# Kernel tuning notes

Hardware: AMD Instinct MI355X
Metric: run time of the kernel (lower is better)

The kernel has to match this reference:

```python
import jax, jax.numpy as jnp
import numpy as np

SQRT_HALF = np.float32(1.0 / np.sqrt(2.0))

# ---------- symmetric-extension index helpers (match dtcwt reflect/symm_pad) ----------

def _reflect(x, minx, maxx):
    rng = maxx - minx
    mod = np.fmod(x - minx, 2 * rng)
    mod = np.where(mod < 0, mod + 2 * rng, mod)
    out = np.where(mod >= rng, 2 * rng - mod, mod) + minx
    return out.astype(np.int64)

def _symm_pad(l, m):
    # indices -m .. l+m-1 reflected with half-sample symmetry (edge repeated)
    return _reflect(np.arange(-m, l + m), -0.5, l - 0.5)

# ---------- 1-D filtering along rows (filters are pre-reversed, so correlation == convolution) ----------

def _corr_rows(X, h):
    # X: (N, C, Hp, W); h: (k,) traced; valid cross-correlation along axis 2
    k = h.shape[0]
    n = X.shape[2] - k + 1
    acc = h[0] * X[:, :, :n, :]
    for t in range(1, k):
        acc = acc + h[t] * X[:, :, t:t + n, :]
    return acc

def colfilter(X, h):
    # level-1 (biort) column filter, symmetric extension, same-size output
    m = h.shape[0] // 2
    xe = _symm_pad(X.shape[2], m)
    return _corr_rows(X[:, :, xe, :], h)

def rowfilter(X, h):
    return jnp.swapaxes(colfilter(jnp.swapaxes(X, 2, 3), h), 2, 3)

def colifilt(X, ha, hb, highpass=False):
    # qshift interpolated column filter: upsample rows by 2 using the (ha, hb) tree pair.
    # Faithful to pytorch_wavelets lowlevel.colifilt (filters stored reversed by prep_filt).
    m = ha.shape[0]
    m2 = m // 2
    r = X.shape[2]  # must be even
    xe = _symm_pad(r, m2)
    hao, hae = ha[1::2], ha[::2]
    hbo, hbe = hb[1::2], hb[::2]
    if m2 % 2 == 0:
        taps = (hae, hbe, hao, hbo)
        if highpass:
            idx = (xe[1:-2:2], xe[:-2:2], xe[3::2], xe[2::2])
        else:
            idx = (xe[:-2:2], xe[1:-2:2], xe[2::2], xe[3::2])
    else:
        taps = (hao, hbo, hae, hbe)
        if highpass:
            idx = (xe[2:-1:2], xe[1:-1:2], xe[2:-1:2], xe[1:-1:2])
        else:
            idx = (xe[1:-1:2], xe[2:-1:2], xe[1:-1:2], xe[2:-1:2])
    ys = [_corr_rows(X[:, :, i, :], h) for i, h in zip(idx, taps)]
    N, C, r2, W = ys[0].shape  # r2 == r // 2
    # interleave the 4 phases -> 2*r rows
    return jnp.stack(ys, axis=3).reshape(N, C, 4 * r2, W)

def rowifilt(X, ha, hb, highpass=False):
    return jnp.swapaxes(colifilt(jnp.swapaxes(X, 2, 3), ha, hb, highpass), 2, 3)


def c2q(w1, w2):
    # w1, w2: (N, C, H, W, 2) -> (N, C, 2H, 2W)
    w1r, w1i = w1[..., 0], w1[..., 1]
    w2r, w2i = w2[..., 0], w2[..., 1]
    a = (w1r + w2r) * SQRT_HALF
    b = (w1i + w2i) * SQRT_HALF
    c = (w1i - w2i) * SQRT_HALF
    d = (w2r - w1r) * SQRT_HALF
    N, C, H, W = a.shape
    top = jnp.stack([a, b], axis=-1).reshape(N, C, H, 2 * W)
    bot = jnp.stack([c, d], axis=-1).reshape(N, C, H, 2 * W)
    return jnp.stack([top, bot], axis=3).reshape(N, C, 2 * H, 2 * W)

# ---------- per-level inverse synthesis ----------

def _inv_j1(ll, yh, g0o, g1o):
    lh = c2q(yh[:, :, 0], yh[:, :, 5])  # 15 / 165 deg
    hl = c2q(yh[:, :, 2], yh[:, :, 3])  # 75 / 105 deg
    hh = c2q(yh[:, :, 1], yh[:, :, 4])  # 45 / 135 deg
    y1 = colfilter(ll, g0o) + colfilter(lh, g1o)
    y2 = colfilter(hl, g0o) + colfilter(hh, g1o)
    return rowfilter(y1, g0o) + rowfilter(y2, g1o)

def _inv_j2plus(ll, yh, g0a, g0b, g1a, g1b):
    lh = c2q(yh[:, :, 0], yh[:, :, 5])
    hl = c2q(yh[:, :, 2], yh[:, :, 3])
    hh = c2q(yh[:, :, 1], yh[:, :, 4])
    y1 = colifilt(ll, g0b, g0a) + colifilt(lh, g1b, g1a, True)
    y2 = colifilt(hl, g0b, g0a) + colifilt(hh, g1b, g1a, True)
    return rowifilt(y1, g0b, g0a) + rowifilt(y2, g1b, g1a, True)

# ---------- filters (near_sym_a biort + qshift_a 10-tap synthesis filters) ----------

def _filters():
    g0o = np.array([-3., -15., 73., 170., 73., -15., -3.]) / 280.0  # 7-tap synthesis lowpass
    g1o = np.array([-1., -5., 12., -5., -1.]) / 20.0                # 5-tap synthesis highpass
    q = np.array([0.03516384, 0.0, -0.08832942, 0.23389032, 0.76027237,
                  0.58751830, 0.0, -0.11430184, 0.0, 0.0])          # 10-tap qshift prototype
    alt = (-1.0) ** np.arange(10)
    g0a, g0b = q[::-1].copy(), q.copy()
    g1a = (alt * q[::-1]).copy()
    g1b = (-alt * q).copy()
    # prep_filt reverses filters so cross-correlation implements true convolution
    f32 = lambda h: jnp.asarray(np.ascontiguousarray(h[::-1]), dtype=jnp.float32)
    return {"g0o": f32(g0o), "g1o": f32(g1o), "g0a": f32(g0a),
            "g0b": f32(g0b), "g1a": f32(g1a), "g1b": f32(g1b)}

def setup_inputs() -> dict:
    key = jax.random.key(0)
    k1, k2, k3, k4 = jax.random.split(key, 4)
    N, C, H = 4, 16, 512  # reconstruct 512x512, J=3
    inp = {
        "yl":  jax.random.normal(k1, (N, C, H // 4, H // 4), jnp.float32),
        "yh0": jax.random.normal(k2, (N, C, 6, H // 2, H // 2, 2), jnp.float32),
        "yh1": jax.random.normal(k3, (N, C, 6, H // 4, H // 4, 2), jnp.float32),
        "yh2": jax.random.normal(k4, (N, C, 6, H // 8, H // 8, 2), jnp.float32),
    }
    inp.update(_filters())
    return inp

def reference(yl, yh0, yh1, yh2, g0o, g1o, g0a, g0b, g1a, g1b):
    ll = _inv_j2plus(yl, yh2, g0a, g0b, g1a, g1b)   # 128 -> 256
    ll = _inv_j2plus(ll, yh1, g0a, g0b, g1a, g1b)   # 256 -> 512
    return _inv_j1(ll, yh0, g0o, g1o)               # 512 -> 512
```

## Files before the change

### kernel.cpp

```cpp
#include <hip/hip_runtime.h>
#include <hip/hip_fp16.h>

#define SQH 0.70710678118654752440f
#define NC 64

typedef float nfloat4 __attribute__((ext_vector_type(4)));

template<int L>
static __device__ __forceinline__ int refl(int i) {
    int j = i & (2 * L - 1);
    return (j >= L) ? (2 * L - 1 - j) : j;
}

static __device__ __forceinline__ void c2q_quad4(float4 A, float4 B,
                                                 float4& p0, float4& p1) {
    p0 = make_float4(SQH * (A.x + B.x), SQH * (A.y + B.y),
                     SQH * (A.z + B.z), SQH * (A.w + B.w));
    p1 = make_float4(SQH * (A.y - B.y), SQH * (B.x - A.x),
                     SQH * (A.w - B.w), SQH * (B.z - A.z));
}

static __device__ __forceinline__ void fma4(float4& a, float s, float4 v) {
    a.x += s * v.x; a.y += s * v.y; a.z += s * v.z; a.w += s * v.w;
}

static __device__ __forceinline__ float4 ld4(const float* p, size_t i4) {
    return ((const float4*)p)[i4];
}
static __device__ __forceinline__ float4 ld4(const __half* p, size_t i4) {
    const __half2* h = (const __half2*)p;
    float2 lo = __half22float2(h[2 * i4]);
    float2 hi = __half22float2(h[2 * i4 + 1]);
    return make_float4(lo.x, lo.y, hi.x, hi.y);
}
static __device__ __forceinline__ void st4(float* p, size_t i4, float4 v) {
    ((float4*)p)[i4] = v;
}
static __device__ __forceinline__ void st4(__half* p, size_t i4, float4 v) {
    __half2* h = (__half2*)p;
    h[2 * i4]     = __float22half2_rn(make_float2(v.x, v.y));
    h[2 * i4 + 1] = __float22half2_rn(make_float2(v.z, v.w));
}

template<int R_, int W_, int TY, typename InT, typename OutT>
__global__ __launch_bounds__(256) void k_i(const InT* __restrict__ ll,
                                           const float* __restrict__ yh,
                                           OutT* __restrict__ out,
                                           const float* __restrict__ g0a, const float* __restrict__ g0b,
                                           const float* __restrict__ g1a, const float* __restrict__ g1b) {
    constexpr int RH = R_ / 2, WH = W_ / 2, WQ = W_ / 4;
    constexpr int SLABS = 2 * R_ / TY;
    constexpr int SW = W_ + 12;
    __shared__ float Y1[TY][SW], Y2[TY][SW];

    constexpr int NBLK = SLABS * NC;
    int bid = blockIdx.x;
    int idx = (bid & 7) * (NBLK >> 3) + (bid >> 3);
    int nc = idx / SLABS, slab = idx % SLABS;
    int nc6 = nc * 6;
    int R0 = slab * TY, i0 = R0 >> 2;
    bool edge = (slab == 0) || (slab == SLABS - 1);

    const InT* llp = ll + (size_t)nc * R_ * W_;
    const float4* yh4 = (const float4*)yh;
    const float4* pHLa = yh4 + (size_t)(nc6 + 2) * RH * WQ;
    const float4* pHLb = yh4 + (size_t)(nc6 + 3) * RH * WQ;
    const float4* pLHa = yh4 + (size_t)(nc6 + 0) * RH * WQ;
    const float4* pLHb = yh4 + (size_t)(nc6 + 5) * RH * WQ;
    const float4* pHHa = yh4 + (size_t)(nc6 + 1) * RH * WQ;
    const float4* pHHb = yh4 + (size_t)(nc6 + 4) * RH * WQ;

    constexpr int ATASK = WQ * (TY / 4);
    for (int task = threadIdx.x; task < ATASK; task += 256) {
        int jq = task & (WQ - 1);
        int gl = task / WQ;
        int i  = i0 + gl;

        float4 a10 = {0,0,0,0}, a20 = {0,0,0,0}, a11 = {0,0,0,0}, a21 = {0,0,0,0};
        float4 a12 = {0,0,0,0}, a22 = {0,0,0,0}, a13 = {0,0,0,0}, a23 = {0,0,0,0};
#pragma unroll
        for (int t = 0; t < 5; ++t) {
            float4 lE, lO, hlE, hlO, lhE, lhO, hhE, hhO;
            if (edge) {
                int rE = refl<R_>(2 * i - 4 + 2 * t);
                int rO = refl<R_>(2 * i - 3 + 2 * t);
                lE = ld4(llp, (size_t)rE * WQ + jq);
                lO = ld4(llp, (size_t)rO * WQ + jq);
                int ii = rE >> 1, diE = rE & 1;
                size_t off = (size_t)ii * WQ + jq;
                float4 p0, p1;
                c2q_quad4(pHLa[off], pHLb[off], p0, p1);
                hlE = diE ? p1 : p0;  hlO = diE ? p0 : p1;
                c2q_quad4(pLHa[off], pLHb[off], p0, p1);
                lhE = diE ? p1 : p0;  lhO = diE ? p0 : p1;
                c2q_quad4(pHHa[off], pHHb[off], p0, p1);
                hhE = diE ? p1 : p0;  hhO = diE ? p0 : p1;
            } else {
                lE = ld4(llp, (size_t)(2 * i - 4 + 2 * t) * WQ + jq);
                lO = ld4(llp, (size_t)(2 * i - 3 + 2 * t) * WQ + jq);
                size_t off = (size_t)(i - 2 + t) * WQ + jq;
                c2q_quad4(pHLa[off], pHLb[off], hlE, hlO);
                c2q_quad4(pLHa[off], pLHb[off], lhE, lhO);
                c2q_quad4(pHHa[off], pHHb[off], hhE, hhO);
            }
            float b0o = g0b[2 * t + 1], a0o = g0a[2 * t + 1];
            float b0e = g0b[2 * t],     a0e = g0a[2 * t];
            float b1o = g1b[2 * t + 1], a1o = g1a[2 * t + 1];
            float b1e = g1b[2 * t],     a1e = g1a[2 * t];
            fma4(a10, b0o, lE);  fma4(a10, b1o, lhO);
            fma4(a20, b0o, hlE); fma4(a20, b1o, hhO);
            fma4(a11, a0o, lO);  fma4(a11, a1o, lhE);
            fma4(a21, a0o, hlO); fma4(a21, a1o, hhE);
            fma4(a12, b0e, lE);  fma4(a12, b1e, lhO);
            fma4(a22, b0e, hlE); fma4(a22, b1e, hhO);
            fma4(a13, a0e, lO);  fma4(a13, a1e, lhE);
            fma4(a23, a0e, hlO); fma4(a23, a1e, hhE);
        }
        int rl = 4 * gl, xc = 4 * jq + 4;
        *(float4*)&Y1[rl + 0][xc] = a10;  *(float4*)&Y2[rl + 0][xc] = a20;
        *(float4*)&Y1[rl + 1][xc] = a11;  *(float4*)&Y2[rl + 1][xc] = a21;
        *(float4*)&Y1[rl + 2][xc] = a12;  *(float4*)&Y2[rl + 2][xc] = a22;
        *(float4*)&Y1[rl + 3][xc] = a13;  *(float4*)&Y2[rl + 3][xc] = a23;
    }
    __syncthreads();

    for (int t = threadIdx.x; t < TY * 9; t += 256) {
        int r = t / 9, h = t % 9;
        int dst, src;
        if (h < 4) { dst = h;              src = 7 - h; }
        else       { int k = h - 4; dst = 4 + W_ + k; src = 4 + W_ - 1 - k; }
        Y1[r][dst] = Y1[r][src];
        Y2[r][dst] = Y2[r][src];
    }
    __syncthreads();

    constexpr int QW = W_ / 2;
    for (int task = threadIdx.x; task < TY * QW; task += 256) {
        int j = task & (QW - 1);
        int r = task / QW;
        float2 v1[5], v2[5];
#pragma unroll
        for (int t = 0; t < 5; ++t) {
            v1[t] = *(const float2*)&Y1[r][2 * j + 2 * t];
            v2[t] = *(const float2*)&Y2[r][2 * j + 2 * t];
        }
        float4 o = make_float4(0.f, 0.f, 0.f, 0.f);
#pragma unroll
        for (int t = 0; t < 5; ++t) {
            float b0o = g0b[2 * t + 1], a0o = g0a[2 * t + 1];
            float b0e = g0b[2 * t],     a0e = g0a[2 * t];
            float b1o = g1b[2 * t + 1], a1o = g1a[2 * t + 1];
            float b1e = g1b[2 * t],     a1e = g1a[2 * t];
            o.x += b0o * v1[t].x + b1o * v2[t].y;
            o.y += a0o * v1[t].y + a1o * v2[t].x;
            o.z += b0e * v1[t].x + b1e * v2[t].y;
            o.w += a0e * v1[t].y + a1e * v2[t].x;
        }
        st4(out, (size_t)(nc * 2 * R_ + R0 + r) * QW + j, o);
    }
}

template<int H, int W, int TY, typename InT>
__global__ __launch_bounds__(256) void k_f0(const InT* __restrict__ ll,
                                            const float* __restrict__ yh,
                                            float* __restrict__ out,
                                            const float* __restrict__ g0o,
                                            const float* __restrict__ g1o) {
    constexpr int RH = H / 2, WH = W / 2, WQ = W / 4;
    constexpr int SLABS = H / TY;
    constexpr int SW = W + 12;
    __shared__ float Y1[TY][SW], Y2[TY][SW];

    constexpr int NBLK = SLABS * NC;
    int bid = blockIdx.x;
    int idx = (bid & 7) * (NBLK >> 3) + (bid >> 3);
    int nc = idx / SLABS, slab = idx % SLABS;
    int nc6 = nc * 6;
    int r0 = slab * TY;
    bool edge = (slab == 0) || (slab == SLABS - 1);

    const InT* llp = ll + (size_t)nc * H * W;
    const float4* yh4 = (const float4*)yh;
    const float4* pHLa = yh4 + (size_t)(nc6 + 2) * RH * WQ;
    const float4* pHLb = yh4 + (size_t)(nc6 + 3) * RH * WQ;
    const float4* pLHa = yh4 + (size_t)(nc6 + 0) * RH * WQ;
    const float4* pLHb = yh4 + (size_t)(nc6 + 5) * RH * WQ;
    const float4* pHHa = yh4 + (size_t)(nc6 + 1) * RH * WQ;
    const float4* pHHb = yh4 + (size_t)(nc6 + 4) * RH * WQ;

    float f0[7], f1[5];
#pragma unroll
    for (int k = 0; k < 7; ++k) f0[k] = g0o[k];
#pragma unroll
    for (int k = 0; k < 5; ++k) f1[k] = g1o[k];

    constexpr int ATASK = WQ * (TY / 4);
    for (int task = threadIdx.x; task < ATASK; task += 256) {
        int jq = task & (WQ - 1);
        int gl = task / WQ;
        int gg = (r0 >> 2) + gl;

        float4 a1[4], a2[4];
#pragma unroll
        for (int q = 0; q < 4; ++q) { a1[q] = make_float4(0,0,0,0); a2[q] = make_float4(0,0,0,0); }

#pragma unroll
        for (int m = 0; m < 10; ++m) {
            float4 v;
            if (edge) v = ld4(llp, (size_t)refl<H>(4 * gg - 3 + m) * WQ + jq);
            else      v = ld4(llp, (size_t)(4 * gg - 3 + m) * WQ + jq);
#pragma unroll
            for (int q = 0; q < 4; ++q)
                if (m - q >= 0 && m - q < 7) fma4(a1[q], f0[m - q], v);
        }
#pragma unroll
        for (int pp = 0; pp < 6; ++pp) {
            float4 vE, vO, p0, p1;
            if (edge) {
                int rE = refl<H>(4 * gg - 4 + 2 * pp);
                int ii = rE >> 1, diE = rE & 1;
                size_t off = (size_t)ii * WQ + jq;
                c2q_quad4(pHLa[off], pHLb[off], p0, p1);
                vE = diE ? p1 : p0;  vO = diE ? p0 : p1;
            } else {
                size_t off = (size_t)(2 * gg - 2 + pp) * WQ + jq;
                c2q_quad4(pHLa[off], pHLb[off], vE, vO);
            }
            if (pp > 0) {
                int m = 2 * pp - 1;
#pragma unroll
                for (int q = 0; q < 4; ++q)
                    if (m - q >= 0 && m - q < 7) fma4(a2[q], f0[m - q], vE);
            }
            if (pp < 5) {
                int m = 2 * pp;
#pragma unroll
                for (int q = 0; q < 4; ++q)
                    if (m - q >= 0 && m - q < 7) fma4(a2[q], f0[m - q], vO);
            }
        }
#pragma unroll
        for (int pp = 0; pp < 4; ++pp) {
            float4 vE, vO, p0, p1;
            size_t off;
            int diE = 0;
            if (edge) {
                int rE = refl<H>(4 * gg - 2 + 2 * pp);
                diE = rE & 1;
                off = (size_t)(rE >> 1) * WQ + jq;
            } else {
                off = (size_t)(2 * gg - 1 + pp) * WQ + jq;
            }
            c2q_quad4(pLHa[off], pLHb[off], p0, p1);
            vE = diE ? p1 : p0;  vO = diE ? p0 : p1;
            {
                int m = 2 * pp;
#pragma unroll
                for (int q = 0; q < 4; ++q)
                    if (m - q >= 0 && m - q < 5) fma4(a1[q], f1[m - q], vE);
            }
            {
                int m = 2 * pp + 1;
#pragma unroll
                for (int q = 0; q < 4; ++q)
                    if (m - q >= 0 && m - q < 5) fma4(a1[q], f1[m - q], vO);
            }
            c2q_quad4(pHHa[off], pHHb[off], p0, p1);
            vE = diE ? p1 : p0;  vO = diE ? p0 : p1;
            {
                int m = 2 * pp;
#pragma unroll
                for (int q = 0; q < 4; ++q)
                    if (m - q >= 0 && m - q < 5) fma4(a2[q], f1[m - q], vE);
            }
            {
                int m = 2 * pp + 1;
#pragma unroll
                for (int q = 0; q < 4; ++q)
                    if (m - q >= 0 && m - q < 5) fma4(a2[q], f1[m - q], vO);
            }
        }
        int rl = 4 * gl, xc = 4 * jq + 4;
#pragma unroll
        for (int q = 0; q < 4; ++q) {
            *(float4*)&Y1[rl + q][xc] = a1[q];
            *(float4*)&Y2[rl + q][xc] = a2[q];
        }
    }
    __syncthreads();

    for (int t = threadIdx.x; t < TY * 9; t += 256) {
        int r = t / 9, h = t % 9;
        int dst, src;
        if (h < 4) { dst = h;              src = 7 - h; }
        else       { int k = h - 4; dst = 4 + W + k; src = 4 + W - 1 - k; }
        Y1[r][dst] = Y1[r][src];
        Y2[r][dst] = Y2[r][src];
    }
    __syncthreads();

    constexpr int QW = W / 4;
    for (int task = threadIdx.x; task < TY * QW; task += 256) {
        int jq = task & (QW - 1);
        int r  = task / QW;
        int c0 = 4 * jq;
        float a[12], b[8];
#pragma unroll
        for (int m = 0; m < 6; ++m) {
            float2 u = *(const float2*)&Y1[r][c0 + 2 * m];
            a[2 * m] = u.x; a[2 * m + 1] = u.y;
        }
#pragma unroll
        for (int m = 0; m < 4; ++m) {
            float2 u = *(const float2*)&Y2[r][c0 + 2 + 2 * m];
            b[2 * m] = u.x; b[2 * m + 1] = u.y;
        }
        float acc[4] = {0.f, 0.f, 0.f, 0.f};
#pragma unroll
        for (int q = 0; q < 4; ++q) {
#pragma unroll
            for (int t = 0; t < 7; ++t) acc[q] += f0[t] * a[q + t + 1];
#pragma unroll
            for (int t = 0; t < 5; ++t) acc[q] += f1[t] * b[q + t];
        }
        nfloat4 nv = {acc[0], acc[1], acc[2], acc[3]};
        __builtin_nontemporal_store(nv,
            (nfloat4*)(out + ((size_t)nc * H + r0 + r) * W + c0));
    }
}

extern "C" void kernel_launch(void* const* d_in, const int* in_sizes, int n_in,
                              void* d_out, int out_size, void* d_ws, size_t ws_size,
                              hipStream_t stream) {
    const float* yl  = (const float*)d_in[0];
    const float* yh0 = (const float*)d_in[1];
    const float* yh1 = (const float*)d_in[2];
    const float* yh2 = (const float*)d_in[3];
    const float* g0o = (const float*)d_in[4];
    const float* g1o = (const float*)d_in[5];
    const float* g0a = (const float*)d_in[6];
    const float* g0b = (const float*)d_in[7];
    const float* g1a = (const float*)d_in[8];
    const float* g1b = (const float*)d_in[9];
    float* out = (float*)d_out;

    char* ws = (char*)d_ws;
    __half* bufA = (__half*)(ws);
    __half* bufB = (__half*)(ws + ((size_t)64 << 20));

    k_i<128, 128, 32, float, __half><<<8 * NC, 256, 0, stream>>>(
        yl, yh2, bufA, g0a, g0b, g1a, g1b);
    k_i<256, 256, 16, __half, __half><<<32 * NC, 256, 0, stream>>>(
        bufA, yh1, bufB, g0a, g0b, g1a, g1b);
    k_f0<512, 512, 8, __half><<<64 * NC, 256, 0, stream>>>(
        bufB, yh0, out, g0o, g1o);
}
```

Baseline: 103.3 us.

## Store intermediate rows as half2 in LDS and compute two row groups per thread

Column-pass intermediates are now kept in shared memory as half2 instead of float. This halves LDS footprint and traffic, and the symmetric-extension padding becomes half2 swaps. Each thread now computes two 4-row groups (GH=2) with sliding loads, so overlapping input rows and highpass rows are reused in registers rather than reloaded. Slab heights double and grid sizes halve to match. This adds fp16 rounding on the intermediates and raises register pressure.

```diff
diff --git a/kernel.cpp b/kernel.cpp
--- a/kernel.cpp
+++ b/kernel.cpp
@@ -42,16 +42,20 @@
     h[2 * i4 + 1] = __float22half2_rn(make_float2(v.z, v.w));
 }
 
-template<int R_, int W_, int TY, typename InT, typename OutT>
+static __device__ __forceinline__ __half2 h2swap(__half2 v) {
+    __half2 r; r.x = v.y; r.y = v.x; return r;
+}
+
+template<int R_, int W_, int TY, int GH, typename InT, typename OutT>
 __global__ __launch_bounds__(256) void k_i(const InT* __restrict__ ll,
                                            const float* __restrict__ yh,
                                            OutT* __restrict__ out,
                                            const float* __restrict__ g0a, const float* __restrict__ g0b,
                                            const float* __restrict__ g1a, const float* __restrict__ g1b) {
-    constexpr int RH = R_ / 2, WH = W_ / 2, WQ = W_ / 4;
+    constexpr int RH = R_ / 2, WQ = W_ / 4, W2 = W_ / 2;
     constexpr int SLABS = 2 * R_ / TY;
-    constexpr int SW = W_ + 12;
-    __shared__ float Y1[TY][SW], Y2[TY][SW];
+    constexpr int SW2 = W2 + 5;
+    __shared__ __half2 Y1h[TY][SW2], Y2h[TY][SW2];
 
     constexpr int NBLK = SLABS * NC;
     int bid = blockIdx.x;
@@ -70,24 +74,26 @@
     const float4* pHHa = yh4 + (size_t)(nc6 + 1) * RH * WQ;
     const float4* pHHb = yh4 + (size_t)(nc6 + 4) * RH * WQ;
 
-    constexpr int ATASK = WQ * (TY / 4);
+    constexpr int ATASK = WQ * (TY / (4 * GH));
     for (int task = threadIdx.x; task < ATASK; task += 256) {
         int jq = task & (WQ - 1);
         int gl = task / WQ;
-        int i  = i0 + gl;
-
-        float4 a10 = {0,0,0,0}, a20 = {0,0,0,0}, a11 = {0,0,0,0}, a21 = {0,0,0,0};
-        float4 a12 = {0,0,0,0}, a22 = {0,0,0,0}, a13 = {0,0,0,0}, a23 = {0,0,0,0};
-#pragma unroll
-        for (int t = 0; t < 5; ++t) {
+        int i  = i0 + GH * gl;
+
+        float4 A1[4 * GH], A2[4 * GH];
+#pragma unroll
+        for (int k = 0; k < 4 * GH; ++k) { A1[k] = make_float4(0,0,0,0); A2[k] = make_float4(0,0,0,0); }
+
+#pragma unroll
+        for (int p = 0; p < 4 + GH; ++p) {
             float4 lE, lO, hlE, hlO, lhE, lhO, hhE, hhO;
             if (edge) {
-                int rE = refl<R_>(2 * i - 4 + 2 * t);
-                int rO = refl<R_>(2 * i - 3 + 2 * t);
+                int rE = refl<R_>(2 * i - 4 + 2 * p);
+                int rO = refl<R_>(2 * i - 3 + 2 * p);
                 lE = ld4(llp, (size_t)rE * WQ + jq);
                 lO = ld4(llp, (size_t)rO * WQ + jq);
-                int ii = rE >> 1, diE = rE & 1;
-                size_t off = (size_t)ii * WQ + jq;
+                int diE = rE & 1;
+                size_t off = (size_t)(rE >> 1) * WQ + jq;
                 float4 p0, p1;
                 c2q_quad4(pHLa[off], pHLb[off], p0, p1);
                 hlE = diE ? p1 : p0;  hlO = diE ? p0 : p1;
@@ -96,41 +102,50 @@
                 c2q_quad4(pHHa[off], pHHb[off], p0, p1);
                 hhE = diE ? p1 : p0;  hhO = diE ? p0 : p1;
             } else {
-                lE = ld4(llp, (size_t)(2 * i - 4 + 2 * t) * WQ + jq);
-                lO = ld4(llp, (size_t)(2 * i - 3 + 2 * t) * WQ + jq);
-                size_t off = (size_t)(i - 2 + t) * WQ + jq;
+                lE = ld4(llp, (size_t)(2 * i - 4 + 2 * p) * WQ + jq);
+                lO = ld4(llp, (size_t)(2 * i - 3 + 2 * p) * WQ + jq);
+                size_t off = (size_t)(i - 2 + p) * WQ + jq;
                 c2q_quad4(pHLa[off], pHLb[off], hlE, hlO);
                 c2q_quad4(pLHa[off], pLHb[off], lhE, lhO);
                 c2q_quad4(pHHa[off], pHHb[off], hhE, hhO);
             }
-            float b0o = g0b[2 * t + 1], a0o = g0a[2 * t + 1];
-            float b0e = g0b[2 * t],     a0e = g0a[2 * t];
-            float b1o = g1b[2 * t + 1], a1o = g1a[2 * t + 1];
-            float b1e = g1b[2 * t],     a1e = g1a[2 * t];
-            fma4(a10, b0o, lE);  fma4(a10, b1o, lhO);
-            fma4(a20, b0o, hlE); fma4(a20, b1o, hhO);
-            fma4(a11, a0o, lO);  fma4(a11, a1o, lhE);
-            fma4(a21, a0o, hlO); fma4(a21, a1o, hhE);
-            fma4(a12, b0e, lE);  fma4(a12, b1e, lhO);
-            fma4(a22, b0e, hlE); fma4(a22, b1e, hhO);
-            fma4(a13, a0e, lO);  fma4(a13, a1e, lhE);
-            fma4(a23, a0e, hlO); fma4(a23, a1e, hhE);
-        }
-        int rl = 4 * gl, xc = 4 * jq + 4;
-        *(float4*)&Y1[rl + 0][xc] = a10;  *(float4*)&Y2[rl + 0][xc] = a20;
-        *(float4*)&Y1[rl + 1][xc] = a11;  *(float4*)&Y2[rl + 1][xc] = a21;
-        *(float4*)&Y1[rl + 2][xc] = a12;  *(float4*)&Y2[rl + 2][xc] = a22;
-        *(float4*)&Y1[rl + 3][xc] = a13;  *(float4*)&Y2[rl + 3][xc] = a23;
+#pragma unroll
+            for (int g = 0; g < GH; ++g) {
+                int t = p - g;
+                if (t >= 0 && t < 5) {
+                    float b0o = g0b[2 * t + 1], a0o = g0a[2 * t + 1];
+                    float b0e = g0b[2 * t],     a0e = g0a[2 * t];
+                    float b1o = g1b[2 * t + 1], a1o = g1a[2 * t + 1];
+                    float b1e = g1b[2 * t],     a1e = g1a[2 * t];
+                    fma4(A1[4*g+0], b0o, lE);  fma4(A1[4*g+0], b1o, lhO);
+                    fma4(A2[4*g+0], b0o, hlE); fma4(A2[4*g+0], b1o, hhO);
+                    fma4(A1[4*g+1], a0o, lO);  fma4(A1[4*g+1], a1o, lhE);
+                    fma4(A2[4*g+1], a0o, hlO); fma4(A2[4*g+1], a1o, hhE);
+                    fma4(A1[4*g+2], b0e, lE);  fma4(A1[4*g+2], b1e, lhO);
+                    fma4(A2[4*g+2], b0e, hlE); fma4(A2[4*g+2], b1e, hhO);
+                    fma4(A1[4*g+3], a0e, lO);  fma4(A1[4*g+3], a1e, lhE);
+                    fma4(A2[4*g+3], a0e, hlO); fma4(A2[4*g+3], a1e, hhE);
+                }
+            }
+        }
+        int rl = 4 * GH * gl, xc2 = 2 * jq + 2;
+#pragma unroll
+        for (int k = 0; k < 4 * GH; ++k) {
+            Y1h[rl + k][xc2]     = __float22half2_rn(make_float2(A1[k].x, A1[k].y));
+            Y1h[rl + k][xc2 + 1] = __float22half2_rn(make_float2(A1[k].z, A1[k].w));
+            Y2h[rl + k][xc2]     = __float22half2_rn(make_float2(A2[k].x, A2[k].y));
+            Y2h[rl + k][xc2 + 1] = __float22half2_rn(make_float2(A2[k].z, A2[k].w));
+        }
     }
     __syncthreads();
 
-    for (int t = threadIdx.x; t < TY * 9; t += 256) {
-        int r = t / 9, h = t % 9;
+    for (int t = threadIdx.x; t < TY * 5; t += 256) {
+        int r = t / 5, h = t % 5;
         int dst, src;
-        if (h < 4) { dst = h;              src = 7 - h; }
-        else       { int k = h - 4; dst = 4 + W_ + k; src = 4 + W_ - 1 - k; }
-        Y1[r][dst] = Y1[r][src];
-        Y2[r][dst] = Y2[r][src];
+        if (h < 2) { dst = h;              src = 3 - h; }
+        else       { int k = h - 2; dst = W2 + 2 + k; src = W2 + 1 - k; }
+        Y1h[r][dst] = h2swap(Y1h[r][src]);
+        Y2h[r][dst] = h2swap(Y2h[r][src]);
     }
     __syncthreads();
 
@@ -141,8 +156,8 @@
         float2 v1[5], v2[5];
 #pragma unroll
         for (int t = 0; t < 5; ++t) {
-            v1[t] = *(const float2*)&Y1[r][2 * j + 2 * t];
-            v2[t] = *(const float2*)&Y2[r][2 * j + 2 * t];
+            v1[t] = __half22float2(Y1h[r][j + t]);
+            v2[t] = __half22float2(Y2h[r][j + t]);
         }
         float4 o = make_float4(0.f, 0.f, 0.f, 0.f);
 #pragma unroll
@@ -166,10 +181,10 @@
                                             float* __restrict__ out,
                                             const float* __restrict__ g0o,
                                             const float* __restrict__ g1o) {
-    constexpr int RH = H / 2, WH = W / 2, WQ = W / 4;
+    constexpr int RH = H / 2, WQ = W / 4, W2 = W / 2;
     constexpr int SLABS = H / TY;
-    constexpr int SW = W + 12;
-    __shared__ float Y1[TY][SW], Y2[TY][SW];
+    constexpr int SW2 = W2 + 5;
+    __shared__ __half2 Y1h[TY][SW2], Y2h[TY][SW2];
 
     constexpr int NBLK = SLABS * NC;
     int bid = blockIdx.x;
@@ -194,108 +209,125 @@
 #pragma unroll
     for (int k = 0; k < 5; ++k) f1[k] = g1o[k];
 
-    constexpr int ATASK = WQ * (TY / 4);
+    constexpr int ATASK = WQ * (TY / 8);
     for (int task = threadIdx.x; task < ATASK; task += 256) {
         int jq = task & (WQ - 1);
         int gl = task / WQ;
-        int gg = (r0 >> 2) + gl;
-
-        float4 a1[4], a2[4];
-#pragma unroll
-        for (int q = 0; q < 4; ++q) { a1[q] = make_float4(0,0,0,0); a2[q] = make_float4(0,0,0,0); }
-
-#pragma unroll
-        for (int m = 0; m < 10; ++m) {
+        int gg = (r0 >> 2) + 2 * gl;
+
+        float4 A1[8], A2[8];
+#pragma unroll
+        for (int k = 0; k < 8; ++k) { A1[k] = make_float4(0,0,0,0); A2[k] = make_float4(0,0,0,0); }
+
+#pragma unroll
+        for (int p = 0; p < 14; ++p) {
             float4 v;
-            if (edge) v = ld4(llp, (size_t)refl<H>(4 * gg - 3 + m) * WQ + jq);
-            else      v = ld4(llp, (size_t)(4 * gg - 3 + m) * WQ + jq);
-#pragma unroll
-            for (int q = 0; q < 4; ++q)
-                if (m - q >= 0 && m - q < 7) fma4(a1[q], f0[m - q], v);
-        }
-#pragma unroll
-        for (int pp = 0; pp < 6; ++pp) {
-            float4 vE, vO, p0, p1;
+            if (edge) v = ld4(llp, (size_t)refl<H>(4 * gg - 3 + p) * WQ + jq);
+            else      v = ld4(llp, (size_t)(4 * gg - 3 + p) * WQ + jq);
+            if (p < 10) {
+#pragma unroll
+                for (int q = 0; q < 4; ++q)
+                    if (p - q >= 0 && p - q < 7) fma4(A1[q], f0[p - q], v);
+            }
+            if (p >= 4) {
+                int m = p - 4;
+#pragma unroll
+                for (int q = 0; q < 4; ++q)
+                    if (m - q >= 0 && m - q < 7) fma4(A1[4 + q], f0[m - q], v);
+            }
+        }
+#pragma unroll
+        for (int P = 0; P < 8; ++P) {
+            float4 vE, vO;
             if (edge) {
-                int rE = refl<H>(4 * gg - 4 + 2 * pp);
-                int ii = rE >> 1, diE = rE & 1;
-                size_t off = (size_t)ii * WQ + jq;
+                int rE = refl<H>(4 * gg - 4 + 2 * P);
+                int diE = rE & 1;
+                size_t off = (size_t)(rE >> 1) * WQ + jq;
+                float4 p0, p1;
                 c2q_quad4(pHLa[off], pHLb[off], p0, p1);
                 vE = diE ? p1 : p0;  vO = diE ? p0 : p1;
             } else {
-                size_t off = (size_t)(2 * gg - 2 + pp) * WQ + jq;
+                size_t off = (size_t)(2 * gg - 2 + P) * WQ + jq;
                 c2q_quad4(pHLa[off], pHLb[off], vE, vO);
             }
-            if (pp > 0) {
-                int m = 2 * pp - 1;
-#pragma unroll
-                for (int q = 0; q < 4; ++q)
-                    if (m - q >= 0 && m - q < 7) fma4(a2[q], f0[m - q], vE);
-            }
-            if (pp < 5) {
-                int m = 2 * pp;
-#pragma unroll
-                for (int q = 0; q < 4; ++q)
-                    if (m - q >= 0 && m - q < 7) fma4(a2[q], f0[m - q], vO);
-            }
-        }
-#pragma unroll
-        for (int pp = 0; pp < 4; ++pp) {
-            float4 vE, vO, p0, p1;
+#pragma unroll
+            for (int g = 0; g < 2; ++g) {
+                int pp = P - 2 * g;
+                if (pp >= 0 && pp <= 5) {
+                    if (pp > 0) {
+                        int m = 2 * pp - 1;
+#pragma unroll
+                        for (int q = 0; q < 4; ++q)
+                            if (m - q >= 0 && m - q < 7) fma4(A2[4*g + q], f0[m - q], vE);
+                    }
+                    if (pp < 5) {
+                        int m = 2 * pp;
+#pragma unroll
+                        for (int q = 0; q < 4; ++q)
+                            if (m - q >= 0 && m - q < 7) fma4(A2[4*g + q], f0[m - q], vO);
+                    }
+                }
+            }
+        }
+#pragma unroll
+        for (int P = 0; P < 6; ++P) {
             size_t off;
             int diE = 0;
             if (edge) {
-                int rE = refl<H>(4 * gg - 2 + 2 * pp);
+                int rE = refl<H>(4 * gg - 2 + 2 * P);
                 diE = rE & 1;
                 off = (size_t)(rE >> 1) * WQ + jq;
             } else {
-                off = (size_t)(2 * gg - 1 + pp) * WQ + jq;
-            }
+                off = (size_t)(2 * gg - 1 + P) * WQ + jq;
+            }
+            float4 p0, p1, vE, vO;
             c2q_quad4(pLHa[off], pLHb[off], p0, p1);
             vE = diE ? p1 : p0;  vO = diE ? p0 : p1;
-            {
-                int m = 2 * pp;
-#pragma unroll
-                for (int q = 0; q < 4; ++q)
-                    if (m - q >= 0 && m - q < 5) fma4(a1[q], f1[m - q], vE);
-            }
-            {
-                int m = 2 * pp + 1;
-#pragma unroll
-                for (int q = 0; q < 4; ++q)
-                    if (m - q >= 0 && m - q < 5) fma4(a1[q], f1[m - q], vO);
+#pragma unroll
+            for (int g = 0; g < 2; ++g) {
+                int pp = P - 2 * g;
+                if (pp >= 0 && pp <= 3) {
+                    int mE = 2 * pp, mO = 2 * pp + 1;
+#pragma unroll
+                    for (int q = 0; q < 4; ++q) {
+                        if (mE - q >= 0 && mE - q < 5) fma4(A1[4*g + q], f1[mE - q], vE);
+                        if (mO - q >= 0 && mO - q < 5) fma4(A1[4*g + q], f1[mO - q], vO);
+                    }
+                }
             }
             c2q_quad4(pHHa[off], pHHb[off], p0, p1);
             vE = diE ? p1 : p0;  vO = diE ? p0 : p1;
-            {
-                int m = 2 * pp;
-#pragma unroll
-                for (int q = 0; q < 4; ++q)
-                    if (m - q >= 0 && m - q < 5) fma4(a2[q], f1[m - q], vE);
-            }
-            {
-                int m = 2 * pp + 1;
-#pragma unroll
-                for (int q = 0; q < 4; ++q)
-                    if (m - q >= 0 && m - q < 5) fma4(a2[q], f1[m - q], vO);
-            }
-        }
-        int rl = 4 * gl, xc = 4 * jq + 4;
-#pragma unroll
-        for (int q = 0; q < 4; ++q) {
-            *(float4*)&Y1[rl + q][xc] = a1[q];
-            *(float4*)&Y2[rl + q][xc] = a2[q];
+#pragma unroll
+            for (int g = 0; g < 2; ++g) {
+                int pp = P - 2 * g;
+                if (pp >= 0 && pp <= 3) {
+                    int mE = 2 * pp, mO = 2 * pp + 1;
+#pragma unroll
+                    for (int q = 0; q < 4; ++q) {
+                        if (mE - q >= 0 && mE - q < 5) fma4(A2[4*g + q], f1[mE - q], vE);
+                        if (mO - q >= 0 && mO - q < 5) fma4(A2[4*g + q], f1[mO - q], vO);
+                    }
+                }
+            }
+        }
+        int rl = 8 * gl, xc2 = 2 * jq + 2;
+#pragma unroll
+        for (int k = 0; k < 8; ++k) {
+            Y1h[rl + k][xc2]     = __float22half2_rn(make_float2(A1[k].x, A1[k].y));
+            Y1h[rl + k][xc2 + 1] = __float22half2_rn(make_float2(A1[k].z, A1[k].w));
+            Y2h[rl + k][xc2]     = __float22half2_rn(make_float2(A2[k].x, A2[k].y));
+            Y2h[rl + k][xc2 + 1] = __float22half2_rn(make_float2(A2[k].z, A2[k].w));
         }
     }
     __syncthreads();
 
-    for (int t = threadIdx.x; t < TY * 9; t += 256) {
-        int r = t / 9, h = t % 9;
+    for (int t = threadIdx.x; t < TY * 5; t += 256) {
+        int r = t / 5, h = t % 5;
         int dst, src;
-        if (h < 4) { dst = h;              src = 7 - h; }
-        else       { int k = h - 4; dst = 4 + W + k; src = 4 + W - 1 - k; }
-        Y1[r][dst] = Y1[r][src];
-        Y2[r][dst] = Y2[r][src];
+        if (h < 2) { dst = h;              src = 3 - h; }
+        else       { int k = h - 2; dst = W2 + 2 + k; src = W2 + 1 - k; }
+        Y1h[r][dst] = h2swap(Y1h[r][src]);
+        Y2h[r][dst] = h2swap(Y2h[r][src]);
     }
     __syncthreads();
 
@@ -303,16 +335,15 @@
     for (int task = threadIdx.x; task < TY * QW; task += 256) {
         int jq = task & (QW - 1);
         int r  = task / QW;
-        int c0 = 4 * jq;
         float a[12], b[8];
 #pragma unroll
         for (int m = 0; m < 6; ++m) {
-            float2 u = *(const float2*)&Y1[r][c0 + 2 * m];
+            float2 u = __half22float2(Y1h[r][2 * jq + m]);
             a[2 * m] = u.x; a[2 * m + 1] = u.y;
         }
 #pragma unroll
         for (int m = 0; m < 4; ++m) {
-            float2 u = *(const float2*)&Y2[r][c0 + 2 + 2 * m];
+            float2 u = __half22float2(Y2h[r][2 * jq + 1 + m]);
             b[2 * m] = u.x; b[2 * m + 1] = u.y;
         }
         float acc[4] = {0.f, 0.f, 0.f, 0.f};
@@ -325,7 +356,7 @@
         }
         nfloat4 nv = {acc[0], acc[1], acc[2], acc[3]};
         __builtin_nontemporal_store(nv,
-            (nfloat4*)(out + ((size_t)nc * H + r0 + r) * W + c0));
+            (nfloat4*)(out + ((size_t)nc * H + r0 + r) * W + 4 * jq));
     }
 }
 
@@ -348,10 +379,10 @@
     __half* bufA = (__half*)(ws);
     __half* bufB = (__half*)(ws + ((size_t)64 << 20));
 
-    k_i<128, 128, 32, float, __half><<<8 * NC, 256, 0, stream>>>(
+    k_i<128, 128, 32, 1, float, __half><<<8 * NC, 256, 0, stream>>>(
         yl, yh2, bufA, g0a, g0b, g1a, g1b);
-    k_i<256, 256, 16, __half, __half><<<32 * NC, 256, 0, stream>>>(
+    k_i<256, 256, 32, 2, __half, __half><<<16 * NC, 256, 0, stream>>>(
         bufA, yh1, bufB, g0a, g0b, g1a, g1b);
-    k_f0<512, 512, 8, __half><<<64 * NC, 256, 0, stream>>>(
+    k_f0<512, 512, 16, __half><<<32 * NC, 256, 0, stream>>>(
         bufB, yh0, out, g0o, g1o);
 }
```

Measured after the change: 105.1 us. Within noise of the previous version (+1.7%).
